# Kernel optimization log

Measured on AMD Instinct MI355X. Metric: run time of the kernel, lower is better.

The kernel has to match this reference:

```python
import jax, jax.numpy as jnp
import numpy as np

B, T, I, H = 128, 1024, 128, 512


def setup_inputs():
    key = jax.random.key(0)
    ks = jax.random.split(key, 7)
    x = jax.random.normal(ks[0], (B, T, I), jnp.float32)
    mask = (jax.random.uniform(ks[1], (B, T)) < 0.1).astype(jnp.int32)
    # lengths sorted DESCENDING (required by the per-step batch truncation); max == T
    length = jnp.sort(jax.random.randint(ks[2], (B,), T // 2, T + 1))[::-1]
    length = length.at[0].set(T)
    s = 1.0 / np.sqrt(H)
    W_ih = jax.random.uniform(ks[3], (4 * H, I), jnp.float32, -s, s)
    W_hh = jax.random.uniform(ks[4], (4 * H, H), jnp.float32, -s, s)
    b_ih = jax.random.uniform(ks[5], (4 * H,), jnp.float32, -s, s)
    b_hh = jax.random.uniform(ks[6], (4 * H,), jnp.float32, -s, s)
    return dict(input=x, mask=mask, length=length, W_ih=W_ih, W_hh=W_hh, b_ih=b_ih, b_hh=b_hh)


def _boundary_mask(mask, length):
    # mask[:,0]=0 then scatter 1 at end index (length-1), as in the torch code
    Bq = mask.shape[0]
    m = mask.astype(jnp.float32)
    m = m.at[:, 0].set(0.0)
    m = m.at[jnp.arange(Bq), length - 1].set(1.0)
    return m


def _gather_index(m):
    # Replicates the pad-to-max-words while-loop + nonzero/gather pipeline.
    # The loop extends a suffix of ones until each row has exactly max_w ones;
    # equivalently: set to 1 every position whose suffix zero-count <= (max_w - num).
    Bq, Tq = m.shape
    word_nums = m.sum(axis=1)
    max_w = word_nums.max()
    need = max_w - word_nums
    zcum = jnp.cumsum((1.0 - m)[:, ::-1], axis=1)[:, ::-1]  # zeros in suffix (inclusive)
    padded = jnp.where(zcum <= need[:, None], 1.0, m)
    K = int(max_w)  # every row now has exactly K ones
    # column indices of the ones, in ascending order (row-major nonzero order)
    cols = jnp.argsort(1.0 - padded, axis=1, stable=True)[:, :K]
    # index = row*T + col - 1, gathered from the flattened embeddings (torch wraps -1)
    flat_idx = (jnp.arange(Bq)[:, None] * Tq + cols - 1) % (Bq * Tq)
    return flat_idx, word_nums, K


def _run_lstm(x, m, active, W_ih, W_hh, b_ih, b_hh):
    # Masked per-timestep LSTMCell: h,c are zeroed at boundaries (mask==0) before
    # each step; rows with t >= length are frozen (emulates batch_size_t truncation
    # for descending-sorted lengths) and their embeddings stay zero.
    Bq = x.shape[0]
    Hq = W_hh.shape[1]
    h0 = jnp.zeros((Bq, Hq), x.dtype)

    def step(carry, xs):
        h, c = carry
        x_t, m_t, a_t = xs
        h = h * m_t[:, None]
        c = c * m_t[:, None]
        gates = x_t @ W_ih.T + h @ W_hh.T + b_ih + b_hh
        i, f, g, o = jnp.split(gates, 4, axis=1)  # torch gate order i,f,g,o
        c2 = jax.nn.sigmoid(f) * c + jax.nn.sigmoid(i) * jnp.tanh(g)
        h2 = jax.nn.sigmoid(o) * jnp.tanh(c2)
        a = a_t[:, None]
        return (a * h2 + (1.0 - a) * h, a * c2 + (1.0 - a) * c), a * h2

    _, emb = jax.lax.scan(step, (h0, h0), (x.transpose(1, 0, 2), m.T, active.T))
    return emb.transpose(1, 0, 2)  # [B, T, H]


def reference(input, mask, length, W_ih, W_hh, b_ih, b_hh):
    Bq, Tq, _ = input.shape
    Hq = W_hh.shape[1]
    m = _boundary_mask(mask, length)
    active = (jnp.arange(Tq)[None, :] < length[:, None]).astype(input.dtype)
    emb = _run_lstm(input, m, active, W_ih, W_hh, b_ih, b_hh)
    flat_idx, word_nums, K = _gather_index(m)
    out = emb.reshape(Bq * Tq, Hq)[flat_idx]  # [B, K, H]
    return out, word_nums
```

## Files before the change

kernel.cpp:

```cpp
#include <hip/hip_runtime.h>
#include <math.h>

#define BB 128
#define TT 1024
#define II 128
#define HH 512
#define GG 2048
#define BT (BB*TT)
#define LMAX 10
#define NBUCK 20

#define BM 128
#define BN 128
#define KCH 128

typedef unsigned short u16;
typedef __attribute__((ext_vector_type(4))) u16 u16x4;
typedef __attribute__((ext_vector_type(8))) u16 u16x8;
typedef __attribute__((ext_vector_type(8))) short bf16x8;
typedef __attribute__((ext_vector_type(4))) float f32x4;

typedef __attribute__((address_space(3))) unsigned int lds_u32;
typedef __attribute__((address_space(1))) const unsigned int gbl_u32;

__device__ __forceinline__ void gload16(const void* g, void* l) {
    __builtin_amdgcn_global_load_lds((gbl_u32*)g, (lds_u32*)l, 16, 0, 0);
}

__device__ __forceinline__ float rcpf(float x) { return __builtin_amdgcn_rcpf(x); }
__device__ __forceinline__ float sigf(float v) { return rcpf(1.0f + __expf(-v)); }
__device__ __forceinline__ float tanhfast(float x) {
    float e = __expf(2.0f * x);
    return 1.0f - 2.0f * rcpf(e + 1.0f);
}

__device__ __forceinline__ u16 f2b(float f) {
    unsigned int x = __float_as_uint(f);
    return (u16)((x + 0x7fffu + ((x >> 16) & 1u)) >> 16);
}

__host__ __device__ __forceinline__ int buck_cap(int bkt, int CAP0) {
    if (bkt == 0) return CAP0;
    if (bkt == 1) return 2048;
    if (bkt == 2) return 256;
    if (bkt <= 9) return 128;
    if (bkt == 10) return 2048;
    if (bkt == 11) return 512;
    if (bkt == 12) return 128;
    return 64;
}
__host__ __device__ __forceinline__ int buck_off(int bkt, int CAP0) {
    int o = 0;
    for (int i = 0; i < bkt; ++i) o += buck_cap(i, CAP0);
    return o;
}
#define LIST_EXTRA (2048 + 256 + 7*128 + 2048 + 512 + 128 + 7*64)

__device__ __forceinline__ int block_scan_excl(int* ws4, int tid, int v, int* total) {
    int lane = tid & 63, wv = tid >> 6;
    int incl = v;
#pragma unroll
    for (int s = 1; s < 64; s <<= 1) {
        int u = __shfl_up(incl, (unsigned)s, 64);
        if (lane >= s) incl += u;
    }
    __syncthreads();
    if (lane == 63) ws4[wv] = incl;
    __syncthreads();
    int base = 0, tot = 0;
#pragma unroll
    for (int i = 0; i < 4; ++i) { int t = ws4[i]; if (i < wv) base += t; tot += t; }
    *total = tot;
    return base + incl - v;
}

__global__ __launch_bounds__(256) void k_prep(
    const int* __restrict__ mask, const int* __restrict__ length,
    const float* __restrict__ x, float* __restrict__ wnOut,
    int* __restrict__ levelCount, int2* __restrict__ levelList,
    int* __restrict__ slotOf, u16* __restrict__ xb, float* __restrict__ out,
    const float* __restrict__ Wih, const float* __restrict__ Whh,
    u16* __restrict__ wihb, u16* __restrict__ whhb,
    int K, int R, int CAP0) {
    int tid = threadIdx.x;
    if (blockIdx.x >= BB) {
        int i = (blockIdx.x - BB) * 256 + tid;
        const int NW = GG * II / 4;
        const int NH = GG * HH / 4;
        if (i < NW) {
            float4 v = ((const float4*)Wih)[i];
            u16x4 u = { f2b(v.x), f2b(v.y), f2b(v.z), f2b(v.w) };
            ((u16x4*)wihb)[i] = u;
        } else if (i < NW + NH) {
            int j = i - NW;
            float4 v = ((const float4*)Whh)[j];
            u16x4 u = { f2b(v.x), f2b(v.y), f2b(v.z), f2b(v.w) };
            ((u16x4*)whhb)[j] = u;
        }
        return;
    }

    __shared__ unsigned char sm[TT];
    __shared__ unsigned char sne[TT];
    __shared__ u16 sgp[TT];
    __shared__ int ws4[4];
    __shared__ int cnt[NBUCK], cnt2[NBUCK], bas[NBUCK], boff[NBUCK];
    __shared__ u16 spos[256];
    __shared__ u16 zlist[256];
    __shared__ int zn;

    int b = blockIdx.x;
    int len = length[b];
    int t0 = tid * 4;
    if (tid == 0) zn = 0;
    if (tid < NBUCK) { cnt[tid] = 0; cnt2[tid] = 0; boff[tid] = buck_off(tid, CAP0); }

    int4 mk = ((const int4*)(mask + (size_t)b * TT))[tid];
    int mraw[4] = { mk.x, mk.y, mk.z, mk.w };
    unsigned char mv[4];
    int lzero = 0;
#pragma unroll
    for (int j = 0; j < 4; ++j) {
        int t = t0 + j;
        unsigned char m = (t == len - 1) ? 1 : ((t == 0) ? 0 : (mraw[j] != 0));
        mv[j] = m;
        sm[t] = m;
        sgp[t] = 0;
        lzero += !m;
    }

    int Z;
    int zbase = block_scan_excl(ws4, tid, lzero, &Z);
    int wn = TT - Z;
    if (tid == 0) wnOut[b] = (float)wn;
    int need = K - wn;

    int psel[4];
    int lpad = 0;
    {
        int zb = zbase;
#pragma unroll
        for (int j = 0; j < 4; ++j) {
            int sel = mv[j] | ((Z - zb) <= need ? 1 : 0);
            psel[j] = sel;
            lpad += sel;
            zb += !mv[j];
        }
    }
    int ptot;
    int pbase = block_scan_excl(ws4, tid, lpad, &ptot);
    {
        int k = pbase;
#pragma unroll
        for (int j = 0; j < 4; ++j) {
            int t = t0 + j;
            if (psel[j]) {
                sgp[t - 1] = (u16)(k + 1);
                if (t - 1 >= len) {
                    int zi = atomicAdd(&zn, 1);
                    if (zi < 256) zlist[zi] = (u16)k;
                }
                ++k;
            }
        }
    }
    __syncthreads();

    int nev[4], lvlv[4];
    int lne = 0;
#pragma unroll
    for (int j = 0; j < 4; ++j) {
        int t = t0 + j;
        int ne = 0;
        if (t < len) {
            int tt = t;
            ne = sgp[tt] != 0;
            while (!ne && tt + 1 < TT && tt + 1 < len && sm[tt + 1]) { ++tt; ne = sgp[tt] != 0; }
        }
        nev[j] = ne;
        sne[t] = (unsigned char)ne;
        lne += ne;
        int l = 0;
        if (mv[j]) { int tt = t; while (tt >= 0 && sm[tt] && l < LMAX - 1) { ++l; --tt; } }
        lvlv[j] = l;
    }

    int ntot;
    int nbase = block_scan_excl(ws4, tid, lne, &ntot);
    {
        int r = nbase;
        int sv[4];
#pragma unroll
        for (int j = 0; j < 4; ++j) {
            if (nev[j]) { sv[j] = b * R + r; if (r < 256) spos[r] = (u16)(t0 + j); }
            else sv[j] = -1;
            r += nev[j];
        }
        *(int4*)(slotOf + (size_t)b * TT + t0) = make_int4(sv[0], sv[1], sv[2], sv[3]);
    }
    __syncthreads();

    int bktv[4];
#pragma unroll
    for (int j = 0; j < 4; ++j) {
        bktv[j] = -1;
        if (nev[j]) {
            int t = t0 + j;
            int pred = (t + 1 < TT) && sm[t + 1] && sne[t + 1];
            int bkt = pred ? (10 + lvlv[j]) : lvlv[j];
            bktv[j] = bkt;
            atomicAdd(&cnt[bkt], 1);
        }
    }
    __syncthreads();
    if (tid < NBUCK) bas[tid] = cnt[tid] ? atomicAdd(&levelCount[tid], cnt[tid]) : 0;
    __syncthreads();
#pragma unroll
    for (int j = 0; j < 4; ++j) if (nev[j]) {
        int t = t0 + j;
        int bkt = bktv[j];
        int r = atomicAdd(&cnt2[bkt], 1);
        int idx = bas[bkt] + r;
        unsigned int y = ((bkt >= 10) ? 0x80000000u : 0u) | (unsigned int)sgp[t];
        if (idx < buck_cap(bkt, CAP0)) levelList[boff[bkt] + idx] = make_int2(b * TT + t, (int)y);
    }
    __syncthreads();

    int nv = (ntot < 256 ? ntot : 256) * 16;
    for (int idx = tid; idx < nv; idx += 256) {
        int r = idx >> 4, part = idx & 15;
        int t = spos[r];
        const float* src = x + ((size_t)b * TT + t) * II + part * 8;
        float4 v0 = ((const float4*)src)[0];
        float4 v1 = ((const float4*)src)[1];
        u16x8 u = { f2b(v0.x), f2b(v0.y), f2b(v0.z), f2b(v0.w),
                    f2b(v1.x), f2b(v1.y), f2b(v1.z), f2b(v1.w) };
        *(u16x8*)(xb + ((size_t)b * R + r) * II + part * 8) = u;
    }
    int znv = zn < 256 ? zn : 256;
    for (int idx = tid; idx < znv * 128; idx += 256) {
        int e = idx >> 7, q = idx & 127;
        ((float4*)(out + ((size_t)b * K + zlist[e]) * HH))[q] = make_float4(0.f, 0.f, 0.f, 0.f);
    }
}

template<int HASH>
__device__ __forceinline__ void gemm_tile(
    const int2* __restrict__ list, int nrow, int jg,
    const u16* __restrict__ xb, const u16* __restrict__ wihb, const u16* __restrict__ whhb,
    const float* __restrict__ bih, const float* __restrict__ bhh,
    const int* __restrict__ slotOf, u16* __restrict__ hb, float* __restrict__ cbuf,
    float* __restrict__ out, int K,
    u16* As, u16* Bs, int* sSlot, int* sPrev, int* sAux) {
    int tid = threadIdx.x;
    if (tid < BM) {
        int2 e = list[(tid < nrow) ? tid : 0];
        int pos = e.x;
        sSlot[tid] = slotOf[pos];
        sPrev[tid] = HASH ? slotOf[pos - 1] : 0;
        unsigned int y = (unsigned int)e.y;
        int grank = (int)(y & 0xFFFFu);
        sAux[tid] = (int)((y & 0x80000000u) | (unsigned int)(grank ? ((pos >> 10) * K + grank) : 0));
    }
    __syncthreads();

    int w = tid >> 6, l = tid & 63;
    int lrow = l >> 4;
    int cbyte = (l & 15) << 4;
    f32x4 acc[2][8];
#pragma unroll
    for (int rb = 0; rb < 2; ++rb)
#pragma unroll
        for (int cb = 0; cb < 8; ++cb) acc[rb][cb] = (f32x4)0.f;

    const int nch = HASH ? 5 : 1;
    for (int kc = 0; kc < nch; ++kc) {
        bool fromX = (kc == 0);
        int koff = kc * KCH - II;
#pragma unroll
        for (int i = 0; i < 8; ++i) {
            int rr = (w << 5) + (i << 2) + lrow;
            int so = cbyte ^ ((rr & 7) << 4);
            const char* srcA = fromX
                ? (const char*)(xb + (size_t)sSlot[rr] * II) + so
                : (const char*)(hb + (size_t)sPrev[rr] * HH + koff) + so;
            gload16(srcA, (char*)As + (w << 13) + (i << 10));
            int gj = (rr >> 5) * HH + jg * 32 + (rr & 31);
            const char* srcB = fromX
                ? (const char*)(wihb + (size_t)gj * II) + so
                : (const char*)(whhb + (size_t)gj * HH + koff) + so;
            gload16(srcB, (char*)Bs + (w << 13) + (i << 10));
        }
        __syncthreads();
#pragma unroll
        for (int s = 0; s < 4; ++s) {
            bf16x8 af[2], bfr[8];
#pragma unroll
            for (int rb = 0; rb < 2; ++rb) {
                int rr = w * 32 + rb * 16 + (l & 15);
                int byte = rr * 256 + ((s * 64 + (l >> 4) * 16) ^ ((rr & 7) << 4));
                af[rb] = *(const bf16x8*)((const char*)As + byte);
            }
#pragma unroll
            for (int cb = 0; cb < 8; ++cb) {
                int rr = cb * 16 + (l & 15);
                int byte = rr * 256 + ((s * 64 + (l >> 4) * 16) ^ ((rr & 7) << 4));
                bfr[cb] = *(const bf16x8*)((const char*)Bs + byte);
            }
#pragma unroll
            for (int rb = 0; rb < 2; ++rb)
#pragma unroll
                for (int cb = 0; cb < 8; ++cb)
                    acc[rb][cb] = __builtin_amdgcn_mfma_f32_16x16x32_bf16(
                        af[rb], bfr[cb], acc[rb][cb], 0, 0, 0);
        }
        if (kc + 1 < nch) __syncthreads();
    }

    int u = l & 15;
    int h0 = jg * 32 + u;
    float b_i[2], b_f[2], b_g[2], b_o[2];
#pragma unroll
    for (int h = 0; h < 2; ++h) {
        int hc = h0 + h * 16;
        b_i[h] = bih[hc] + bhh[hc];
        b_f[h] = bih[HH + hc] + bhh[HH + hc];
        b_g[h] = bih[2 * HH + hc] + bhh[2 * HH + hc];
        b_o[h] = bih[3 * HH + hc] + bhh[3 * HH + hc];
    }
#pragma unroll
    for (int rb = 0; rb < 2; ++rb) {
#pragma unroll
        for (int r = 0; r < 4; ++r) {
            int m = w * 32 + rb * 16 + (l >> 4) * 4 + r;
            if (m < nrow) {
                int aux = sAux[m];
                int oi = aux & 0x7FFFFFFF;
                int sp = HASH ? sPrev[m] : 0;
                int sl = sSlot[m];
#pragma unroll
                for (int h = 0; h < 2; ++h) {
                    int hc = h0 + h * 16;
                    float gi = acc[rb][0 + h][r] + b_i[h];
                    float gf = acc[rb][2 + h][r] + b_f[h];
                    float gg = acc[rb][4 + h][r] + b_g[h];
                    float go = acc[rb][6 + h][r] + b_o[h];
                    float cin = HASH ? cbuf[(size_t)sp * HH + hc] : 0.f;
                    float c2 = sigf(gf) * cin + sigf(gi) * tanhfast(gg);
                    float h2 = sigf(go) * tanhfast(c2);
                    if (oi) out[(size_t)(oi - 1) * HH + hc] = h2;
                    if (aux < 0) {
                        hb[(size_t)sl * HH + hc] = f2b(h2);
                        cbuf[(size_t)sl * HH + hc] = c2;
                    }
                }
            }
        }
    }
}

template<int HASH>
__global__ __launch_bounds__(256) void k_dual(
    int bktA, int offA, int capA, int ntA,
    int bktB, int offB, int capB, int ntTot,
    const int* __restrict__ levelCount, const int2* __restrict__ levelList,
    const u16* __restrict__ xb, const u16* __restrict__ wihb, const u16* __restrict__ whhb,
    const float* __restrict__ bih, const float* __restrict__ bhh,
    const int* __restrict__ slotOf, u16* __restrict__ hb, float* __restrict__ cbuf,
    float* __restrict__ out, int K) {
    __shared__ __align__(16) u16 As[BM * KCH];
    __shared__ __align__(16) u16 Bs[BN * KCH];
    __shared__ int sSlot[BM], sPrev[BM], sAux[BM];
    int bid = (int)blockIdx.x;
    int xcd = bid & 7, q = bid >> 3;
    int jg = q & 15;
    int v = ((q >> 4) << 3) + xcd;
    if (v >= ntTot) return;
    const int2* lst;
    int n, base;
    if (v < ntA) {
        n = levelCount[bktA]; if (n > capA) n = capA;
        base = v * BM;
        lst = levelList + offA;
    } else {
        n = levelCount[bktB]; if (n > capB) n = capB;
        base = (v - ntA) * BM;
        lst = levelList + offB;
    }
    if (base >= n) return;
    gemm_tile<HASH>(lst + base, min(BM, n - base), jg,
                    xb, wihb, whhb, bih, bhh, slotOf, hb, cbuf, out, K,
                    As, Bs, sSlot, sPrev, sAux);
}

__global__ __launch_bounds__(256) void k_tail39(
    int CAP0, const int* __restrict__ levelCount, const int2* __restrict__ levelList,
    const u16* __restrict__ xb, const u16* __restrict__ wihb, const u16* __restrict__ whhb,
    const float* __restrict__ bih, const float* __restrict__ bhh,
    const int* __restrict__ slotOf, u16* __restrict__ hb, float* __restrict__ cbuf,
    float* __restrict__ out, int K, int* __restrict__ bar) {
    __shared__ __align__(16) u16 As[BM * KCH];
    __shared__ __align__(16) u16 Bs[BN * KCH];
    __shared__ int sSlot[BM], sPrev[BM], sAux[BM];
    int tid = threadIdx.x;
    int iter = 0;
    for (int l = 3; l <= 9; ++l) {
        int bkt = (blockIdx.x == 0) ? (10 + l) : l;
        int cap = buck_cap(bkt, CAP0);
        int n = levelCount[bkt]; if (n > cap) n = cap;
        if (n > 0) {
            gemm_tile<1>(levelList + buck_off(bkt, CAP0), min(BM, n), blockIdx.y,
                         xb, wihb, whhb, bih, bhh, slotOf, hb, cbuf, out, K,
                         As, Bs, sSlot, sPrev, sAux);
        }
        int rem = 0;
        for (int j = l + 1; j <= 9; ++j) {
            int a = levelCount[10 + j]; if (a > buck_cap(10 + j, CAP0)) a = buck_cap(10 + j, CAP0);
            int c = levelCount[j];      if (c > buck_cap(j, CAP0))      c = buck_cap(j, CAP0);
            rem += a + c;
        }
        ++iter;
        if (rem == 0) return;
        __threadfence();
        __syncthreads();
        if (tid == 0) {
            __hip_atomic_fetch_add(bar, 1, __ATOMIC_RELEASE, __HIP_MEMORY_SCOPE_AGENT);
            int target = 32 * iter;
            while (__hip_atomic_load(bar, __ATOMIC_ACQUIRE, __HIP_MEMORY_SCOPE_AGENT) < target) {
                __builtin_amdgcn_s_sleep(1);
            }
        }
        __syncthreads();
        __threadfence();
    }
}

extern "C" void kernel_launch(void* const* d_in, const int* in_sizes, int n_in,
                              void* d_out, int out_size, void* d_ws, size_t ws_size,
                              hipStream_t stream) {
    const float* x    = (const float*)d_in[0];
    const int* mask   = (const int*)d_in[1];
    const int* length = (const int*)d_in[2];
    const float* Wih  = (const float*)d_in[3];
    const float* Whh  = (const float*)d_in[4];
    const float* bih  = (const float*)d_in[5];
    const float* bhh  = (const float*)d_in[6];
    float* out = (float*)d_out;

    int K = (out_size - BB) / (BB * HH);
    int R = K + 64;
    int SLOTS = BB * R;
    int CAP0 = SLOTS;

    char* basep = (char*)d_ws;
    size_t off = 0;
    auto take = [&](size_t bytes) -> char* {
        off = (off + 255) & ~(size_t)255;
        char* p = basep + off;
        off += bytes;
        return p;
    };
    int* slotOf      = (int*)take((size_t)BT * 4);
    int* levelCount  = (int*)take((NBUCK + 1) * 4);
    int2* levelList  = (int2*)take((size_t)(CAP0 + LIST_EXTRA) * 8);
    u16* xb          = (u16*)take((size_t)SLOTS * II * 2);
    u16* hb          = (u16*)take((size_t)SLOTS * HH * 2);
    float* cbuf      = (float*)take((size_t)SLOTS * HH * 4);
    u16* wihb        = (u16*)take((size_t)GG * II * 2);
    u16* whhb        = (u16*)take((size_t)GG * HH * 2);
    int* bar         = levelCount + NBUCK;
    (void)ws_size; (void)in_sizes; (void)n_in;

    hipMemsetAsync(levelCount, 0, (NBUCK + 1) * 4, stream);

    const int NWCVT = (GG * (II + HH) / 4 + 255) / 256;
    k_prep<<<BB + NWCVT, 256, 0, stream>>>(
        mask, length, x, out + (size_t)BB * K * HH,
        levelCount, levelList, slotOf, xb, out, Wih, Whh, wihb, whhb, K, R, CAP0);

    {
        int oS = buck_off(10, CAP0), cS = buck_cap(10, CAP0);
        int ntS = (cS + BM - 1) / BM;
        int ntTot = ntS + (CAP0 + BM - 1) / BM;
        int nv8 = (ntTot + 7) & ~7;
        k_dual<0><<<dim3(nv8 * 16, 1), 256, 0, stream>>>(
            10, oS, cS, ntS, 0, 0, CAP0, ntTot, levelCount, levelList,
            xb, wihb, whhb, bih, bhh, slotOf, hb, cbuf, out, K);
    }
    for (int l = 1; l <= 2; ++l) {
        int oS = buck_off(10 + l, CAP0), cS = buck_cap(10 + l, CAP0);
        int oL = buck_off(l, CAP0),      cL = buck_cap(l, CAP0);
        int ntS = (cS + BM - 1) / BM;
        int ntTot = ntS + (cL + BM - 1) / BM;
        int nv8 = (ntTot + 7) & ~7;
        k_dual<1><<<dim3(nv8 * 16, 1), 256, 0, stream>>>(
            10 + l, oS, cS, ntS, l, oL, cL, ntTot, levelCount, levelList,
            xb, wihb, whhb, bih, bhh, slotOf, hb, cbuf, out, K);
    }
    k_tail39<<<dim3(2, 16), 256, 0, stream>>>(
        CAP0, levelCount, levelList, xb, wihb, whhb, bih, bhh,
        slotOf, hb, cbuf, out, K, bar);
}
```

Measured before the change: 89.63 us.

## Specialize level-0 kernel as persistent x-only GEMM and fold level 2 into tail

Adds a dedicated level-0 kernel that skips the W_hh/h part, since the state is zero at word starts. It loads the W_ih tile into LDS once per block and loops persistently over work units on a capped grid. The level-2 launch is removed and handled inside the grid-barrier tail kernel, which now uses three blocks in x so the long-bucket level can take two tiles. This cuts one kernel launch and redundant weight loads, at the cost of one more barrier iteration and more blocks spinning on the barrier.

```diff
diff --git a/kernel.cpp b/kernel.cpp
--- a/kernel.cpp
+++ b/kernel.cpp
@@ -352,6 +352,142 @@
                     if (aux < 0) {
                         hb[(size_t)sl * HH + hc] = f2b(h2);
                         cbuf[(size_t)sl * HH + hc] = c2;
+                    }
+                }
+            }
+        }
+    }
+}
+
+__global__ __launch_bounds__(256) void k_dual0(
+    int offS, int capS, int ntS, int CAP0, int ntTot, int nUnits,
+    const int* __restrict__ levelCount, const int2* __restrict__ levelList,
+    const u16* __restrict__ xb, const u16* __restrict__ wihb,
+    const float* __restrict__ bih, const float* __restrict__ bhh,
+    const int* __restrict__ slotOf, u16* __restrict__ hb, float* __restrict__ cbuf,
+    float* __restrict__ out, int K) {
+    __shared__ __align__(16) u16 As[BM * KCH];
+    __shared__ __align__(16) u16 Bs[BN * KCH];
+    __shared__ int sSlot[BM], sAux[BM];
+    int tid = threadIdx.x;
+    int w = tid >> 6, l = tid & 63;
+    int lrow = l >> 4;
+    int cbyte = (l & 15) << 4;
+    int jg = ((int)blockIdx.x >> 3) & 15;
+
+#pragma unroll
+    for (int i = 0; i < 8; ++i) {
+        int sp = (w << 3) + i;
+        int rr = (sp << 2) + lrow;
+        int so = cbyte ^ ((rr & 7) << 4);
+        int gj = (rr >> 5) * HH + jg * 32 + (rr & 31);
+        gload16((const char*)(wihb + (size_t)gj * II) + so, (char*)Bs + (sp << 10));
+    }
+
+    int u = l & 15;
+    int h0 = jg * 32 + u;
+    float b_i[2], b_f[2], b_g[2], b_o[2];
+#pragma unroll
+    for (int h = 0; h < 2; ++h) {
+        int hc = h0 + h * 16;
+        b_i[h] = bih[hc] + bhh[hc];
+        b_f[h] = bih[HH + hc] + bhh[HH + hc];
+        b_g[h] = bih[2 * HH + hc] + bhh[2 * HH + hc];
+        b_o[h] = bih[3 * HH + hc] + bhh[3 * HH + hc];
+    }
+
+    for (int unit = (int)blockIdx.x; unit < nUnits; unit += (int)gridDim.x) {
+        int xcd = unit & 7, q = unit >> 3;
+        int v = ((q >> 4) << 3) + xcd;
+        if (v >= ntTot) continue;
+        const int2* lst;
+        int n, base;
+        if (v < ntS) {
+            n = levelCount[10]; if (n > capS) n = capS;
+            base = v * BM;
+            lst = levelList + offS;
+        } else {
+            n = levelCount[0]; if (n > CAP0) n = CAP0;
+            base = (v - ntS) * BM;
+            lst = levelList;
+        }
+        if (base >= n) continue;
+        int nrow = min(BM, n - base);
+        lst += base;
+
+        __syncthreads();
+        if (tid < BM) {
+            int2 e = lst[(tid < nrow) ? tid : 0];
+            int pos = e.x;
+            sSlot[tid] = slotOf[pos];
+            unsigned int y = (unsigned int)e.y;
+            int grank = (int)(y & 0xFFFFu);
+            sAux[tid] = (int)((y & 0x80000000u) |
+                              (unsigned int)(grank ? ((pos >> 10) * K + grank) : 0));
+        }
+        __syncthreads();
+
+#pragma unroll
+        for (int i = 0; i < 8; ++i) {
+            int rr = (w << 5) + (i << 2) + lrow;
+            int so = cbyte ^ ((rr & 7) << 4);
+            gload16((const char*)(xb + (size_t)sSlot[rr] * II) + so,
+                    (char*)As + (w << 13) + (i << 10));
+        }
+        __syncthreads();
+
+        f32x4 acc[2][8];
+#pragma unroll
+        for (int rb = 0; rb < 2; ++rb)
+#pragma unroll
+            for (int cb = 0; cb < 8; ++cb) acc[rb][cb] = (f32x4)0.f;
+#pragma unroll
+        for (int s = 0; s < 4; ++s) {
+            bf16x8 af[2], bfr[8];
+#pragma unroll
+            for (int rb = 0; rb < 2; ++rb) {
+                int rr = w * 32 + rb * 16 + (l & 15);
+                int byte = rr * 256 + ((s * 64 + (l >> 4) * 16) ^ ((rr & 7) << 4));
+                af[rb] = *(const bf16x8*)((const char*)As + byte);
+            }
+#pragma unroll
+            for (int cb = 0; cb < 8; ++cb) {
+                int rr = cb * 16 + (l & 15);
+                int byte = rr * 256 + ((s * 64 + (l >> 4) * 16) ^ ((rr & 7) << 4));
+                bfr[cb] = *(const bf16x8*)((const char*)Bs + byte);
+            }
+#pragma unroll
+            for (int rb = 0; rb < 2; ++rb)
+#pragma unroll
+                for (int cb = 0; cb < 8; ++cb)
+                    acc[rb][cb] = __builtin_amdgcn_mfma_f32_16x16x32_bf16(
+                        af[rb], bfr[cb], acc[rb][cb], 0, 0, 0);
+        }
+
+#pragma unroll
+        for (int rb = 0; rb < 2; ++rb) {
+#pragma unroll
+            for (int r = 0; r < 4; ++r) {
+                int m = w * 32 + rb * 16 + (l >> 4) * 4 + r;
+                if (m < nrow) {
+                    int aux = sAux[m];
+                    int oi = aux & 0x7FFFFFFF;
+                    int sl = sSlot[m];
+#pragma unroll
+                    for (int h = 0; h < 2; ++h) {
+                        int hc = h0 + h * 16;
+                        float gi = acc[rb][0 + h][r] + b_i[h];
+                        float gf = acc[rb][2 + h][r] + b_f[h];
+                        float gg = acc[rb][4 + h][r] + b_g[h];
+                        float go = acc[rb][6 + h][r] + b_o[h];
+                        float c2 = sigf(gi) * tanhfast(gg) * 1.0f;
+                        c2 = sigf(gf) * 0.f + c2;
+                        float h2 = sigf(go) * tanhfast(c2);
+                        if (oi) out[(size_t)(oi - 1) * HH + hc] = h2;
+                        if (aux < 0) {
+                            hb[(size_t)sl * HH + hc] = f2b(h2);
+                            cbuf[(size_t)sl * HH + hc] = c2;
+                        }
                     }
                 }
             }
@@ -393,7 +529,7 @@
                     As, Bs, sSlot, sPrev, sAux);
 }
 
-__global__ __launch_bounds__(256) void k_tail39(
+__global__ __launch_bounds__(256) void k_tail29(
     int CAP0, const int* __restrict__ levelCount, const int2* __restrict__ levelList,
     const u16* __restrict__ xb, const u16* __restrict__ wihb, const u16* __restrict__ whhb,
     const float* __restrict__ bih, const float* __restrict__ bhh,
@@ -404,14 +540,17 @@
     __shared__ int sSlot[BM], sPrev[BM], sAux[BM];
     int tid = threadIdx.x;
     int iter = 0;
-    for (int l = 3; l <= 9; ++l) {
-        int bkt = (blockIdx.x == 0) ? (10 + l) : l;
+    for (int l = 2; l <= 9; ++l) {
+        int bkt, tile;
+        if (blockIdx.x == 0) { bkt = 10 + l; tile = 0; }
+        else { bkt = l; tile = (int)blockIdx.x - 1; }
         int cap = buck_cap(bkt, CAP0);
         int n = levelCount[bkt]; if (n > cap) n = cap;
-        if (n > 0) {
-            gemm_tile<1>(levelList + buck_off(bkt, CAP0), min(BM, n), blockIdx.y,
-                         xb, wihb, whhb, bih, bhh, slotOf, hb, cbuf, out, K,
-                         As, Bs, sSlot, sPrev, sAux);
+        int base = tile * BM;
+        if (base < n) {
+            gemm_tile<1>(levelList + buck_off(bkt, CAP0) + base, min(BM, n - base),
+                         blockIdx.y, xb, wihb, whhb, bih, bhh, slotOf, hb, cbuf,
+                         out, K, As, Bs, sSlot, sPrev, sAux);
         }
         int rem = 0;
         for (int j = l + 1; j <= 9; ++j) {
@@ -425,7 +564,7 @@
         __syncthreads();
         if (tid == 0) {
             __hip_atomic_fetch_add(bar, 1, __ATOMIC_RELEASE, __HIP_MEMORY_SCOPE_AGENT);
-            int target = 32 * iter;
+            int target = 48 * iter;
             while (__hip_atomic_load(bar, __ATOMIC_ACQUIRE, __HIP_MEMORY_SCOPE_AGENT) < target) {
                 __builtin_amdgcn_s_sleep(1);
             }
@@ -483,21 +622,23 @@
         int ntS = (cS + BM - 1) / BM;
         int ntTot = ntS + (CAP0 + BM - 1) / BM;
         int nv8 = (ntTot + 7) & ~7;
-        k_dual<0><<<dim3(nv8 * 16, 1), 256, 0, stream>>>(
-            10, oS, cS, ntS, 0, 0, CAP0, ntTot, levelCount, levelList,
-            xb, wihb, whhb, bih, bhh, slotOf, hb, cbuf, out, K);
-    }
-    for (int l = 1; l <= 2; ++l) {
-        int oS = buck_off(10 + l, CAP0), cS = buck_cap(10 + l, CAP0);
-        int oL = buck_off(l, CAP0),      cL = buck_cap(l, CAP0);
+        int nUnits = nv8 * 16;
+        int grid = nUnits < 512 ? nUnits : 512;
+        k_dual0<<<dim3(grid, 1), 256, 0, stream>>>(
+            oS, cS, ntS, CAP0, ntTot, nUnits, levelCount, levelList,
+            xb, wihb, bih, bhh, slotOf, hb, cbuf, out, K);
+    }
+    {
+        int oS = buck_off(11, CAP0), cS = buck_cap(11, CAP0);
+        int oL = buck_off(1, CAP0),  cL = buck_cap(1, CAP0);
         int ntS = (cS + BM - 1) / BM;
         int ntTot = ntS + (cL + BM - 1) / BM;
         int nv8 = (ntTot + 7) & ~7;
         k_dual<1><<<dim3(nv8 * 16, 1), 256, 0, stream>>>(
-            10 + l, oS, cS, ntS, l, oL, cL, ntTot, levelCount, levelList,
+            11, oS, cS, ntS, 1, oL, cL, ntTot, levelCount, levelList,
             xb, wihb, whhb, bih, bhh, slotOf, hb, cbuf, out, K);
     }
-    k_tail39<<<dim3(2, 16), 256, 0, stream>>>(
+    k_tail29<<<dim3(3, 16), 256, 0, stream>>>(
         CAP0, levelCount, levelList, xb, wihb, whhb, bih, bhh,
         slotOf, hb, cbuf, out, K, bar);
 }
```

Result: slower. 97.51 us (+8.8%).
